# Kernel tuning notes

Hardware: AMD Instinct MI355X
Metric: run time of the kernel (lower is better)

Reference implementation:

```python
import jax, jax.numpy as jnp
import numpy as np

D_FEATURE = 1024
HEAD = 16
D_K = 64
D_V = 64
EPS = 1e-6


def setup_inputs() -> dict:
    key = jax.random.key(0)
    ks = jax.random.split(key, 12)
    B, S = 2, 2048
    s_in = 1.0 / np.sqrt(D_FEATURE)
    s_o = 1.0 / np.sqrt(HEAD * D_V)
    return {
        "q": jax.random.normal(ks[0], (B, S, D_FEATURE), jnp.float32),
        "k": jax.random.normal(ks[1], (B, S, D_FEATURE), jnp.float32),
        "v": jax.random.normal(ks[2], (B, S, D_FEATURE), jnp.float32),
        "Wq": jax.random.uniform(ks[3], (D_FEATURE, HEAD * D_K), jnp.float32, -s_in, s_in),
        "bq": jnp.zeros((HEAD * D_K,), jnp.float32),
        "Wk": jax.random.uniform(ks[4], (D_FEATURE, HEAD * D_K), jnp.float32, -s_in, s_in),
        "bk": jnp.zeros((HEAD * D_K,), jnp.float32),
        "Wv": jax.random.uniform(ks[5], (D_FEATURE, HEAD * D_V), jnp.float32, -s_in, s_in),
        "bv": jnp.zeros((HEAD * D_V,), jnp.float32),
        "Wo": jax.random.uniform(ks[6], (HEAD * D_V, D_FEATURE), jnp.float32, -s_o, s_o),
        "bo": jnp.zeros((D_FEATURE,), jnp.float32),
        "gamma": jnp.ones((D_FEATURE,), jnp.float32),
        "beta": jnp.zeros((D_FEATURE,), jnp.float32),
    }


def reference(q, k, v, Wq, bq, Wk, bk, Wv, bv, Wo, bo, gamma, beta):
    B, Sq, _ = q.shape
    Sk, Sv = k.shape[1], v.shape[1]
    shortcut = v
    # projections -> (b, h, s, d)
    qh = (q @ Wq + bq).reshape(B, Sq, HEAD, D_K).transpose(0, 2, 1, 3)
    kh = (k @ Wk + bk).reshape(B, Sk, HEAD, D_K).transpose(0, 2, 1, 3)
    vh = (v @ Wv + bv).reshape(B, Sv, HEAD, D_V).transpose(0, 2, 1, 3)
    scale = 1.0 / np.sqrt(D_K).astype(np.float32)
    scores = jnp.einsum('bhqd,bhkd->bhqk', qh * scale, kh)
    attn = jax.nn.softmax(scores, axis=-1)  # dropout is identity (p=0 / eval)
    ctx = jnp.einsum('bhqk,bhkd->bhqd', attn, vh)
    ctx = ctx.transpose(0, 2, 1, 3).reshape(B, Sv, HEAD * D_V)
    out = ctx @ Wo + bo
    out = out + shortcut
    # LayerNorm, eps=1e-6
    mu = out.mean(-1, keepdims=True)
    var = out.var(-1, keepdims=True)
    out = (out - mu) * jax.lax.rsqrt(var + EPS) * gamma + beta
    return out
```

## Files before the change

### kernel.cpp

```cpp
#include <hip/hip_runtime.h>

#define D_FEAT 1024
#define NTOK   4096
#define SEQ    2048
#define NHEAD  16
#define DK     64
#define QSCALE 0.1803368801111204f

typedef float          f32x4  __attribute__((ext_vector_type(4)));
typedef float          f32x16 __attribute__((ext_vector_type(16)));
typedef short          s16x8  __attribute__((ext_vector_type(8)));
typedef unsigned short u16x4  __attribute__((ext_vector_type(4)));

__device__ __forceinline__ unsigned short f2bf(float f) {
  union { float f; unsigned int u; } x; x.f = f;
  unsigned int r = x.u + 0x7fffu + ((x.u >> 16) & 1u);
  return (unsigned short)(r >> 16);
}
__device__ __forceinline__ unsigned short f2h(float f) {
  union { _Float16 h; unsigned short u; } x; x.h = (_Float16)f; return x.u;
}
__device__ __forceinline__ float h2f(unsigned short u) {
  union { _Float16 h; unsigned short u; } x; x.u = u; return (float)x.h;
}

__device__ __forceinline__ f32x4 mfma16(s16x8 a, s16x8 b, f32x4 c) {
  return __builtin_amdgcn_mfma_f32_16x16x32_bf16(a, b, c, 0, 0, 0);
}
__device__ __forceinline__ f32x16 mfma32(s16x8 a, s16x8 b, f32x16 c) {
  return __builtin_amdgcn_mfma_f32_32x32x16_bf16(a, b, c, 0, 0, 0);
}

__device__ __forceinline__ void gload16(const void* g, void* l) {
  __builtin_amdgcn_global_load_lds(
      (const __attribute__((address_space(1))) void*)g,
      (__attribute__((address_space(3))) void*)l, 16, 0, 0);
}

__device__ __forceinline__ float fexp2(float x) {
  return __builtin_amdgcn_exp2f(x);
}

__device__ __forceinline__ unsigned int cvtpk(float a, float b) {
  unsigned int r;
  asm("v_cvt_pk_bf16_f32 %0, %1, %2" : "=v"(r) : "v"(a), "v"(b));
  return r;
}
__device__ __forceinline__ void swap32(unsigned int& x, unsigned int& y) {
  asm("v_permlane32_swap_b32 %0, %1" : "+v"(x), "+v"(y));
}
__device__ __forceinline__ s16x8 mk8(unsigned int a, unsigned int b,
                                     unsigned int c, unsigned int d) {
  union { unsigned int u[4]; s16x8 v; } x;
  x.u[0] = a; x.u[1] = b; x.u[2] = c; x.u[3] = d; return x.v;
}

__global__ __launch_bounds__(256) void prep_kernel(
    const float* __restrict__ q, const float* __restrict__ k, const float* __restrict__ v,
    const float* __restrict__ Wq, const float* __restrict__ Wk,
    const float* __restrict__ Wv, const float* __restrict__ Wo,
    unsigned short* __restrict__ qb, unsigned short* __restrict__ kb,
    unsigned short* __restrict__ vb,
    unsigned short* __restrict__ WT, unsigned short* __restrict__ Wot)
{
  __shared__ float tile[32][33];
  const int bx = blockIdx.x, tid = threadIdx.x;
  if (bx < 12288) {
    int sel = bx >> 12;
    const float* src = sel == 0 ? q : (sel == 1 ? k : v);
    unsigned short* dst = sel == 0 ? qb : (sel == 1 ? kb : vb);
    size_t i = ((size_t)(bx & 4095) * 256 + tid) * 4;
    float4 f = *(const float4*)(src + i);
    u16x4 o; o.x = f2bf(f.x); o.y = f2bf(f.y); o.z = f2bf(f.z); o.w = f2bf(f.w);
    *(u16x4*)(dst + i) = o;
  } else {
    int t = bx - 12288;
    int z = t >> 10, rest = t & 1023;
    int bxt = rest & 31, byt = rest >> 5;
    const float* W = z == 0 ? Wq : z == 1 ? Wk : z == 2 ? Wv : Wo;
    unsigned short* T = (z < 3) ? (WT + (size_t)z * 1024 * 1024) : Wot;
    int tx = tid & 31, ty = tid >> 5;
    int n = bxt * 32 + tx;
    for (int i = 0; i < 4; ++i) {
      int kk = byt * 32 + ty + i * 8;
      tile[ty + i * 8][tx] = W[(size_t)kk * D_FEAT + n];
    }
    __syncthreads();
    int kk = byt * 32 + tx;
    for (int i = 0; i < 4; ++i) {
      int n2 = bxt * 32 + ty + i * 8;
      T[(size_t)n2 * D_FEAT + kk] = f2bf(tile[tx][ty + i * 8]);
    }
  }
}

__global__ __launch_bounds__(256, 3) void gemm_qkv(
    const unsigned short* __restrict__ qb, const unsigned short* __restrict__ kb,
    const unsigned short* __restrict__ vb, const unsigned short* __restrict__ WT,
    const float* __restrict__ bq, const float* __restrict__ bk, const float* __restrict__ bv,
    unsigned short* __restrict__ Qp, unsigned short* __restrict__ Kp, unsigned short* __restrict__ Vt)
{
  __shared__ __align__(16) unsigned short sAB[2 * 128 * 64];
  unsigned short* sA = sAB;
  unsigned short* sB = sAB + 128 * 64;
  const int tid = threadIdx.x;
  const int wave = tid >> 6, lane = tid & 63;
  const int quad = lane >> 4, l16 = lane & 15;
  const int wx = wave & 1, wy = wave >> 1;
  const int bx = blockIdx.x;
  const int chunk = bx >> 3;

  const unsigned short* rA;
  const unsigned short* rB;
  int m0, n0;
  if (chunk < 2) {
    m0 = blockIdx.y * 128; n0 = (bx & 7) * 128;
    rA = (chunk ? kb : qb) + (size_t)m0 * D_FEAT;
    rB = WT + (size_t)(chunk * 1024 + n0) * D_FEAT;
  } else {
    m0 = (bx & 7) * 128; n0 = blockIdx.y * 128;
    rA = WT + (size_t)(2048 + m0) * D_FEAT;
    rB = vb + (size_t)n0 * D_FEAT;
  }

  f32x4 acc[4][4];
  for (int mt = 0; mt < 4; ++mt)
    for (int nt = 0; nt < 4; ++nt) acc[mt][nt] = (f32x4){0.f, 0.f, 0.f, 0.f};

  const int rw8 = lane >> 3;
  const int cls = ((lane & 7) ^ (lane >> 3)) * 8;
  const int sw = l16 & 7;

  for (int k0 = 0; k0 < D_FEAT; k0 += 64) {
    __syncthreads();
    for (int j = 0; j < 4; ++j) {
      int ch = wave * 4 + j;
      gload16(rA + (size_t)(ch * 8 + rw8) * D_FEAT + k0 + cls, sA + ch * 512);
      gload16(rB + (size_t)(ch * 8 + rw8) * D_FEAT + k0 + cls, sB + ch * 512);
    }
    __syncthreads();
    s16x8 af[2][4], bfr[2][4];
    for (int kk = 0; kk < 2; ++kk) {
      int c = ((kk * 4 + quad) ^ sw) * 8;
      for (int mt = 0; mt < 4; ++mt)
        af[kk][mt] = *(const s16x8*)(sA + (wy * 64 + mt * 16 + l16) * 64 + c);
      for (int nt = 0; nt < 4; ++nt)
        bfr[kk][nt] = *(const s16x8*)(sB + (wx * 64 + nt * 16 + l16) * 64 + c);
    }
    for (int kk = 0; kk < 2; ++kk)
      for (int mt = 0; mt < 4; ++mt)
        for (int nt = 0; nt < 4; ++nt)
          acc[mt][nt] = mfma16(af[kk][mt], bfr[kk][nt], acc[mt][nt]);
  }

  if (chunk < 2) {
    const float* bias = chunk ? bk : bq;
    unsigned short* Cp = chunk ? Kp : Qp;
    const float scale = chunk == 0 ? QSCALE : 1.0f;
    for (int mt = 0; mt < 4; ++mt)
      for (int nt = 0; nt < 4; ++nt) {
        int col = n0 + wx * 64 + nt * 16 + l16;
        float bcol = bias[col];
        for (int r = 0; r < 4; ++r) {
          int row = m0 + wy * 64 + mt * 16 + quad * 4 + r;
          Cp[(size_t)row * D_FEAT + col] = f2bf((acc[mt][nt][r] + bcol) * scale);
        }
      }
  } else {
    for (int mt = 0; mt < 4; ++mt)
      for (int r = 0; r < 4; ++r) {
        float bfeat = bv[m0 + wy * 64 + mt * 16 + quad * 4 + r];
        for (int nt = 0; nt < 4; ++nt) acc[mt][nt][r] += bfeat;
      }
    unsigned short* tb = sAB;
    for (int p = 0; p < 2; ++p) {
      __syncthreads();
      if (wx == p) {
        for (int mt = 0; mt < 4; ++mt)
          for (int nt = 0; nt < 4; ++nt) {
            int tok_loc = nt * 16 + l16;
            for (int r = 0; r < 4; ++r) {
              int f_loc = wy * 64 + mt * 16 + quad * 4 + r;
              tb[f_loc * 72 + tok_loc] = f2bf(acc[mt][nt][r]);
            }
          }
      }
      __syncthreads();
      int n_base = n0 + p * 64;
      int b = n_base >> 11, tok0 = n_base & 2047;
      int ck = lane & 7;
      for (int j = 0; j < 4; ++j) {
        int f_loc = (wave * 4 + j) * 8 + rw8;
        int f = m0 + f_loc, hh = f >> 6, dv = f & 63;
        *(s16x8*)(Vt + ((size_t)(b * 16 + hh) * 64 + dv) * SEQ + tok0 + ck * 8) =
            *(const s16x8*)(tb + f_loc * 72 + ck * 8);
      }
    }
  }
}

__global__ __launch_bounds__(256) void gemm_o(
    const unsigned short* __restrict__ A, const unsigned short* __restrict__ Bt,
    const float* __restrict__ bias, const float* __restrict__ resid,
    float* __restrict__ Cout)
{
  __shared__ __align__(16) unsigned short sA[128 * 64];
  __shared__ __align__(16) unsigned short sB[64 * 64];
  const int tid = threadIdx.x;
  const int wave = tid >> 6, lane = tid & 63;
  const int quad = lane >> 4, l16 = lane & 15;
  const int wx = wave & 1, wy = wave >> 1;
  const int n0 = blockIdx.x * 64, m0 = blockIdx.y * 128;

  f32x4 acc[4][2];
  for (int mt = 0; mt < 4; ++mt)
    for (int nt = 0; nt < 2; ++nt) acc[mt][nt] = (f32x4){0.f, 0.f, 0.f, 0.f};

  const int rw8 = lane >> 3;
  const int cls = ((lane & 7) ^ (lane >> 3)) * 8;
  const int sw = l16 & 7;

  for (int k0 = 0; k0 < D_FEAT; k0 += 64) {
    __syncthreads();
    for (int j = 0; j < 4; ++j) {
      int ch = wave * 4 + j;
      gload16(A + (size_t)(m0 + ch * 8 + rw8) * D_FEAT + k0 + cls, sA + ch * 512);
    }
    for (int j = 0; j < 2; ++j) {
      int ch = wave * 2 + j;
      gload16(Bt + (size_t)(n0 + ch * 8 + rw8) * D_FEAT + k0 + cls, sB + ch * 512);
    }
    __syncthreads();
    s16x8 af[2][4], bfr[2][2];
    for (int kk = 0; kk < 2; ++kk) {
      int c = ((kk * 4 + quad) ^ sw) * 8;
      for (int mt = 0; mt < 4; ++mt)
        af[kk][mt] = *(const s16x8*)(sA + (wy * 64 + mt * 16 + l16) * 64 + c);
      for (int nt = 0; nt < 2; ++nt)
        bfr[kk][nt] = *(const s16x8*)(sB + (wx * 32 + nt * 16 + l16) * 64 + c);
    }
    for (int kk = 0; kk < 2; ++kk)
      for (int mt = 0; mt < 4; ++mt)
        for (int nt = 0; nt < 2; ++nt)
          acc[mt][nt] = mfma16(af[kk][mt], bfr[kk][nt], acc[mt][nt]);
  }

  for (int mt = 0; mt < 4; ++mt)
    for (int nt = 0; nt < 2; ++nt) {
      int col = n0 + wx * 32 + nt * 16 + l16;
      float bcol = bias[col];
      for (int r = 0; r < 4; ++r) {
        int row = m0 + wy * 64 + mt * 16 + quad * 4 + r;
        Cout[(size_t)row * D_FEAT + col] =
            acc[mt][nt][r] + bcol + resid[(size_t)row * D_FEAT + col];
      }
    }
}

__global__ __launch_bounds__(256, 3) void flash_part(
    const unsigned short* __restrict__ Qp,
    const unsigned short* __restrict__ Kp,
    const unsigned short* __restrict__ Vt,
    unsigned short* __restrict__ Opart,
    float* __restrict__ L)
{
  __shared__ __align__(16) unsigned short sB4[4][4096];

  const int tid = threadIdx.x;
  const int wave = tid >> 6, lane = tid & 63;
  const int l32 = lane & 31, h = lane >> 5;

  const int blk = blockIdx.x;
  const int xcd = blk & 7, jj = blk >> 3;
  const int grp = xcd * 8 + (jj >> 4);
  const int q0 = (jj & 15) * 128;
  const int bh = grp & 31, z = grp >> 5;
  const int b = bh >> 4, hd = bh & 15;
  const int kbase = z * (SEQ / 2);
  const size_t base = (size_t)b * SEQ * D_FEAT + (size_t)hd * DK;
  const unsigned short* vt = Vt + (size_t)bh * 64 * SEQ;

  const int qrow = wave * 32 + l32;

  const unsigned short* qptr = Qp + base + (size_t)(q0 + qrow) * D_FEAT;
  s16x8 bq[4];
#pragma unroll
  for (int s = 0; s < 4; ++s)
    bq[s] = *(const s16x8*)(qptr + (2 * s + h) * 8);

  const int krow = tid >> 3;
  const unsigned short* kPtr =
      Kp + base + (size_t)(kbase + krow) * D_FEAT + (((tid & 7) ^ (krow & 7)) * 8);
  const int vrow = tid >> 2;
  const unsigned short* vPtr =
      vt + (size_t)vrow * SEQ + kbase + (((tid & 3) ^ ((tid >> 3) & 3)) * 8);

  const int kdst = wave * 512;
#pragma unroll
  for (int pb = 0; pb < 2; ++pb) {
    gload16(kPtr, &sB4[pb][kdst]);
    gload16(vPtr, &sB4[pb][2048 + kdst]);
    kPtr += 32 * D_FEAT; vPtr += 32;
  }

  f32x16 o0, o1, stE, stO;
#pragma unroll
  for (int r = 0; r < 16; ++r) { o0[r] = 0.f; o1[r] = 0.f; }
  float lsA = 0.f, lsB = 0.f;

  const int kxor = l32 & 7;
  const int vxor = (l32 >> 1) & 3;

#define QK_TILE(BUF, ST)                                                       \
  {                                                                            \
    const unsigned short* bK = &sB4[BUF][0];                                   \
    _Pragma("unroll") for (int r = 0; r < 16; ++r) ST[r] = 0.f;                \
    __builtin_amdgcn_s_setprio(1);                                            \
    _Pragma("unroll") for (int s = 0; s < 4; ++s) {                            \
      s16x8 a = *(const s16x8*)(bK + l32 * 64 + (((2 * s + h) ^ kxor) * 8));   \
      ST = mfma32(a, bq[s], ST);                                               \
    }                                                                          \
    __builtin_amdgcn_s_setprio(0);                                            \
  }

#define SMPV_TILE(BUFV, ST)                                                    \
  {                                                                            \
    const unsigned short* bV = &sB4[BUFV][2048];                               \
    unsigned int c[8];                                                         \
    _Pragma("unroll") for (int i = 0; i < 8; ++i) {                            \
      float e0 = fexp2(ST[2 * i]);                                             \
      float e1 = fexp2(ST[2 * i + 1]);                                         \
      lsA += e0; lsB += e1;                                                    \
      c[i] = cvtpk(e0, e1);                                                    \
    }                                                                          \
    swap32(c[0], c[2]); swap32(c[1], c[3]);                                    \
    swap32(c[4], c[6]); swap32(c[5], c[7]);                                    \
    s16x8 bp0 = mk8(c[0], c[1], c[2], c[3]);                  \
    s16x8 bp1 = mk8(c[4], c[5], c[6], c[7]);                  \
    __builtin_amdgcn_s_setprio(1);                                            \
    _Pragma("unroll") for (int kk = 0; kk < 2; ++kk) {                         \
      int cs = ((2 * kk + h) ^ vxor) * 8;                                      \
      s16x8 av0 = *(const s16x8*)(bV + l32 * 32 + cs);                         \
      s16x8 av1 = *(const s16x8*)(bV + (32 + l32) * 32 + cs);                  \
      s16x8 bp = kk ? bp1 : bp0;                                               \
      o0 = mfma32(av0, bp, o0);                                                \
      o1 = mfma32(av1, bp, o1);                                                \
    }                                                                          \
    __builtin_amdgcn_s_setprio(0);                                            \
  }

#define SYNC2                                                                  \
  asm volatile("s_waitcnt vmcnt(2)" ::: "memory");                             \
  __builtin_amdgcn_s_barrier();                                               \
  __builtin_amdgcn_sched_barrier(0);
#define ISSUE(NXT)                                                             \
  gload16(kPtr, &sB4[NXT][kdst]);                                              \
  gload16(vPtr, &sB4[NXT][2048 + kdst]);                                       \
  kPtr += 32 * D_FEAT; vPtr += 32;

  SYNC2; ISSUE(2); QK_TILE(0, stE);
  SYNC2; ISSUE(3); QK_TILE(1, stO); SMPV_TILE(0, stE);
  SYNC2; ISSUE(0); QK_TILE(2, stE); SMPV_TILE(1, stO);
  SYNC2; ISSUE(1); QK_TILE(3, stO); SMPV_TILE(2, stE);
  for (int g6 = 0; g6 < 6; ++g6) {
    SYNC2; ISSUE(2); QK_TILE(0, stE); SMPV_TILE(3, stO);
    SYNC2; ISSUE(3); QK_TILE(1, stO); SMPV_TILE(0, stE);
    SYNC2; ISSUE(0); QK_TILE(2, stE); SMPV_TILE(1, stO);
    SYNC2; ISSUE(1); QK_TILE(3, stO); SMPV_TILE(2, stE);
  }
  SYNC2; ISSUE(2); QK_TILE(0, stE); SMPV_TILE(3, stO);
  SYNC2; ISSUE(3); QK_TILE(1, stO); SMPV_TILE(0, stE);
  SYNC2;           QK_TILE(2, stE); SMPV_TILE(1, stO);
  asm volatile("s_waitcnt vmcnt(0)" ::: "memory");
  __builtin_amdgcn_s_barrier();
  __builtin_amdgcn_sched_barrier(0);
  QK_TILE(3, stO); SMPV_TILE(2, stE);
  SMPV_TILE(3, stO);
#undef QK_TILE
#undef SMPV_TILE
#undef SYNC2
#undef ISSUE

  float lsum = lsA + lsB;
  lsum += __shfl_xor(lsum, 32, 64);
  const size_t trow = (size_t)(z * 32 + bh) * SEQ + (q0 + qrow);
  unsigned short* orow = Opart + trow * 64;
#pragma unroll
  for (int g = 0; g < 4; ++g) {
    u16x4 ov;
    for (int r = 0; r < 4; ++r) ov[r] = f2h(o0[4 * g + r]);
    *(u16x4*)(orow + 8 * g + 4 * h) = ov;
  }
#pragma unroll
  for (int g = 0; g < 4; ++g) {
    u16x4 ov;
    for (int r = 0; r < 4; ++r) ov[r] = f2h(o1[4 * g + r]);
    *(u16x4*)(orow + 32 + 8 * g + 4 * h) = ov;
  }
  if (h == 0) L[trow] = lsum;
}

__global__ __launch_bounds__(256) void combine_kernel(
    const unsigned short* __restrict__ Opart, const float* __restrict__ L,
    unsigned short* __restrict__ ctx)
{
  const int idx = blockIdx.x * 256 + threadIdx.x;
  const int dq = idx & 15;
  const int trow = idx >> 4;
  const int bh = trow >> 11, tok = trow & 2047;
  const int b = bh >> 4, h = bh & 15;
  const int HS = 32 * SEQ;

  float inv = __builtin_amdgcn_rcpf(L[trow] + L[HS + trow]);

  u16x4 p0 = *(const u16x4*)(Opart + (size_t)trow * 64 + dq * 4);
  u16x4 p1 = *(const u16x4*)(Opart + ((size_t)HS + trow) * 64 + dq * 4);
  u16x4 o;
  for (int r = 0; r < 4; ++r)
    o[r] = f2bf((h2f(p0[r]) + h2f(p1[r])) * inv);
  *(u16x4*)(ctx + (size_t)b * SEQ * D_FEAT + (size_t)tok * D_FEAT + h * 64 + dq * 4) = o;
}

__global__ __launch_bounds__(256) void ln_kernel(
    const float* __restrict__ x, const float* __restrict__ gamma,
    const float* __restrict__ beta, float* __restrict__ out)
{
  const int row = blockIdx.x, tid = threadIdx.x;
  const int wave = tid >> 6, lane = tid & 63;
  const float* xr = x + (size_t)row * D_FEAT;
  float4 v = ((const float4*)xr)[tid];
  float s  = v.x + v.y + v.z + v.w;
  float ss = v.x * v.x + v.y * v.y + v.z * v.z + v.w * v.w;
  for (int off = 1; off < 64; off <<= 1) {
    s  += __shfl_xor(s,  off, 64);
    ss += __shfl_xor(ss, off, 64);
  }
  __shared__ float red[8];
  if (lane == 0) { red[wave] = s; red[wave + 4] = ss; }
  __syncthreads();
  s  = red[0] + red[1] + red[2] + red[3];
  ss = red[4] + red[5] + red[6] + red[7];
  float mean = s * (1.f / D_FEAT);
  float var  = ss * (1.f / D_FEAT) - mean * mean;
  float rstd = rsqrtf(var + 1e-6f);
  float4 g  = ((const float4*)gamma)[tid];
  float4 bt = ((const float4*)beta)[tid];
  float4 o;
  o.x = (v.x - mean) * rstd * g.x + bt.x;
  o.y = (v.y - mean) * rstd * g.y + bt.y;
  o.z = (v.z - mean) * rstd * g.z + bt.z;
  o.w = (v.w - mean) * rstd * g.w + bt.w;
  ((float4*)(out + (size_t)row * D_FEAT))[tid] = o;
}

extern "C" void kernel_launch(void* const* d_in, const int* in_sizes, int n_in,
                              void* d_out, int out_size, void* d_ws, size_t ws_size,
                              hipStream_t stream) {
  const float* q     = (const float*)d_in[0];
  const float* k     = (const float*)d_in[1];
  const float* v     = (const float*)d_in[2];
  const float* Wq    = (const float*)d_in[3];
  const float* bq    = (const float*)d_in[4];
  const float* Wk    = (const float*)d_in[5];
  const float* bk    = (const float*)d_in[6];
  const float* Wv    = (const float*)d_in[7];
  const float* bv    = (const float*)d_in[8];
  const float* Wo    = (const float*)d_in[9];
  const float* bo    = (const float*)d_in[10];
  const float* gamma = (const float*)d_in[11];
  const float* beta  = (const float*)d_in[12];

  char* w = (char*)d_ws;
  const size_t MB = 1u << 20;
  unsigned short* qb    = (unsigned short*)(w + 0 * MB);
  unsigned short* kb    = (unsigned short*)(w + 8 * MB);
  unsigned short* vb    = (unsigned short*)(w + 16 * MB);
  unsigned short* WT    = (unsigned short*)(w + 24 * MB);
  unsigned short* Wot   = (unsigned short*)(w + 30 * MB);
  unsigned short* Qp    = (unsigned short*)(w + 32 * MB);
  unsigned short* Kp    = (unsigned short*)(w + 40 * MB);
  unsigned short* Vt    = (unsigned short*)(w + 48 * MB);
  unsigned short* ctx   = (unsigned short*)(w + 56 * MB);
  float*          tmp   = (float*)(w + 64 * MB);
  unsigned short* Opart = (unsigned short*)(w + 0 * MB);
  float*          L     = (float*)(w + 16 * MB);

  prep_kernel<<<16384, 256, 0, stream>>>(q, k, v, Wq, Wk, Wv, Wo, qb, kb, vb, WT, Wot);

  gemm_qkv<<<dim3(24, 32), 256, 0, stream>>>(qb, kb, vb, WT, bq, bk, bv, Qp, Kp, Vt);

  flash_part<<<1024, 256, 0, stream>>>(Qp, Kp, Vt, Opart, L);

  combine_kernel<<<4096, 256, 0, stream>>>(Opart, L, ctx);

  gemm_o<<<dim3(16, 32), 256, 0, stream>>>(ctx, Wot, bo, v, tmp);

  ln_kernel<<<NTOK, 256, 0, stream>>>(tmp, gamma, beta, (float*)d_out);
}
```

Baseline: 230.2 us.

## Double-buffer LDS tiles in QKV and output projection GEMMs

Both the QKV projection and output projection GEMMs now keep two LDS buffers. The global-to-LDS loads for the next K tile are issued while the current tile is being computed, and partial vmcnt waits replace full __syncthreads pairs. The aim is to hide global load latency behind MFMA work. In exchange, shared memory per block doubles, and the QKV kernel's launch bound drops from 3 to 2 blocks per CU, which reduces occupancy.

```diff
diff --git a/kernel.cpp b/kernel.cpp
--- a/kernel.cpp
+++ b/kernel.cpp
@@ -94,15 +94,13 @@
   }
 }
 
-__global__ __launch_bounds__(256, 3) void gemm_qkv(
+__global__ __launch_bounds__(256, 2) void gemm_qkv(
     const unsigned short* __restrict__ qb, const unsigned short* __restrict__ kb,
     const unsigned short* __restrict__ vb, const unsigned short* __restrict__ WT,
     const float* __restrict__ bq, const float* __restrict__ bk, const float* __restrict__ bv,
     unsigned short* __restrict__ Qp, unsigned short* __restrict__ Kp, unsigned short* __restrict__ Vt)
 {
-  __shared__ __align__(16) unsigned short sAB[2 * 128 * 64];
-  unsigned short* sA = sAB;
-  unsigned short* sB = sAB + 128 * 64;
+  __shared__ __align__(16) unsigned short sAB[2][2 * 128 * 64];
   const int tid = threadIdx.x;
   const int wave = tid >> 6, lane = tid & 63;
   const int quad = lane >> 4, l16 = lane & 15;
@@ -131,27 +129,59 @@
   const int cls = ((lane & 7) ^ (lane >> 3)) * 8;
   const int sw = l16 & 7;
 
-  for (int k0 = 0; k0 < D_FEAT; k0 += 64) {
-    __syncthreads();
-    for (int j = 0; j < 4; ++j) {
-      int ch = wave * 4 + j;
-      gload16(rA + (size_t)(ch * 8 + rw8) * D_FEAT + k0 + cls, sA + ch * 512);
-      gload16(rB + (size_t)(ch * 8 + rw8) * D_FEAT + k0 + cls, sB + ch * 512);
-    }
-    __syncthreads();
-    s16x8 af[2][4], bfr[2][4];
-    for (int kk = 0; kk < 2; ++kk) {
-      int c = ((kk * 4 + quad) ^ sw) * 8;
-      for (int mt = 0; mt < 4; ++mt)
-        af[kk][mt] = *(const s16x8*)(sA + (wy * 64 + mt * 16 + l16) * 64 + c);
-      for (int nt = 0; nt < 4; ++nt)
-        bfr[kk][nt] = *(const s16x8*)(sB + (wx * 64 + nt * 16 + l16) * 64 + c);
-    }
-    for (int kk = 0; kk < 2; ++kk)
-      for (int mt = 0; mt < 4; ++mt)
-        for (int nt = 0; nt < 4; ++nt)
-          acc[mt][nt] = mfma16(af[kk][mt], bfr[kk][nt], acc[mt][nt]);
-  }
+#define QKV_ISSUE(BUF, K0)                                                     \
+  _Pragma("unroll") for (int j = 0; j < 4; ++j) {                              \
+    int ch = wave * 4 + j;                                                     \
+    gload16(rA + (size_t)(ch * 8 + rw8) * D_FEAT + (K0) + cls,                 \
+            &sAB[BUF][ch * 512]);                                              \
+    gload16(rB + (size_t)(ch * 8 + rw8) * D_FEAT + (K0) + cls,                 \
+            &sAB[BUF][128 * 64 + ch * 512]);                                   \
+  }
+
+#define QKV_COMP(BUF)                                                         \
+  {                                                                            \
+    const unsigned short* sA = &sAB[BUF][0];                                   \
+    const unsigned short* sB = &sAB[BUF][128 * 64];                            \
+    s16x8 af[2][4], bfr[2][4];                                                 \
+    _Pragma("unroll") for (int kk = 0; kk < 2; ++kk) {                         \
+      int c = ((kk * 4 + quad) ^ sw) * 8;                                      \
+      _Pragma("unroll") for (int mt = 0; mt < 4; ++mt)                         \
+        af[kk][mt] = *(const s16x8*)(sA + (wy * 64 + mt * 16 + l16) * 64 + c); \
+      _Pragma("unroll") for (int nt = 0; nt < 4; ++nt)                         \
+        bfr[kk][nt] = *(const s16x8*)(sB + (wx * 64 + nt * 16 + l16) * 64 + c);\
+    }                                                                          \
+    _Pragma("unroll") for (int kk = 0; kk < 2; ++kk)                           \
+      _Pragma("unroll") for (int mt = 0; mt < 4; ++mt)                         \
+        _Pragma("unroll") for (int nt = 0; nt < 4; ++nt)                       \
+          acc[mt][nt] = mfma16(af[kk][mt], bfr[kk][nt], acc[mt][nt]);          \
+  }
+
+#define GSYNC(N)                                                               \
+  asm volatile("s_waitcnt vmcnt(" #N ")" ::: "memory");                        \
+  __builtin_amdgcn_s_barrier();                                               \
+  __builtin_amdgcn_sched_barrier(0);
+
+  QKV_ISSUE(0, 0);
+  QKV_ISSUE(1, 64);
+  for (int t2 = 0; t2 < 14; t2 += 2) {
+    GSYNC(8);
+    QKV_COMP(0);
+    __builtin_amdgcn_s_barrier();
+    __builtin_amdgcn_sched_barrier(0);
+    QKV_ISSUE(0, (t2 + 2) * 64);
+    GSYNC(8);
+    QKV_COMP(1);
+    __builtin_amdgcn_s_barrier();
+    __builtin_amdgcn_sched_barrier(0);
+    QKV_ISSUE(1, (t2 + 3) * 64);
+  }
+  GSYNC(8);
+  QKV_COMP(0);
+  GSYNC(0);
+  QKV_COMP(1);
+#undef QKV_ISSUE
+#undef QKV_COMP
+#undef GSYNC
 
   if (chunk < 2) {
     const float* bias = chunk ? bk : bq;
@@ -172,7 +202,7 @@
         float bfeat = bv[m0 + wy * 64 + mt * 16 + quad * 4 + r];
         for (int nt = 0; nt < 4; ++nt) acc[mt][nt][r] += bfeat;
       }
-    unsigned short* tb = sAB;
+    unsigned short* tb = &sAB[0][0];
     for (int p = 0; p < 2; ++p) {
       __syncthreads();
       if (wx == p) {
@@ -204,8 +234,8 @@
     const float* __restrict__ bias, const float* __restrict__ resid,
     float* __restrict__ Cout)
 {
-  __shared__ __align__(16) unsigned short sA[128 * 64];
-  __shared__ __align__(16) unsigned short sB[64 * 64];
+  __shared__ __align__(16) unsigned short sA2[2][128 * 64];
+  __shared__ __align__(16) unsigned short sB2[2][64 * 64];
   const int tid = threadIdx.x;
   const int wave = tid >> 6, lane = tid & 63;
   const int quad = lane >> 4, l16 = lane & 15;
@@ -220,30 +250,62 @@
   const int cls = ((lane & 7) ^ (lane >> 3)) * 8;
   const int sw = l16 & 7;
 
-  for (int k0 = 0; k0 < D_FEAT; k0 += 64) {
-    __syncthreads();
-    for (int j = 0; j < 4; ++j) {
-      int ch = wave * 4 + j;
-      gload16(A + (size_t)(m0 + ch * 8 + rw8) * D_FEAT + k0 + cls, sA + ch * 512);
-    }
-    for (int j = 0; j < 2; ++j) {
-      int ch = wave * 2 + j;
-      gload16(Bt + (size_t)(n0 + ch * 8 + rw8) * D_FEAT + k0 + cls, sB + ch * 512);
-    }
-    __syncthreads();
-    s16x8 af[2][4], bfr[2][2];
-    for (int kk = 0; kk < 2; ++kk) {
-      int c = ((kk * 4 + quad) ^ sw) * 8;
-      for (int mt = 0; mt < 4; ++mt)
-        af[kk][mt] = *(const s16x8*)(sA + (wy * 64 + mt * 16 + l16) * 64 + c);
-      for (int nt = 0; nt < 2; ++nt)
-        bfr[kk][nt] = *(const s16x8*)(sB + (wx * 32 + nt * 16 + l16) * 64 + c);
-    }
-    for (int kk = 0; kk < 2; ++kk)
-      for (int mt = 0; mt < 4; ++mt)
-        for (int nt = 0; nt < 2; ++nt)
-          acc[mt][nt] = mfma16(af[kk][mt], bfr[kk][nt], acc[mt][nt]);
-  }
+#define O_ISSUE(BUF, K0)                                                       \
+  _Pragma("unroll") for (int j = 0; j < 4; ++j) {                              \
+    int ch = wave * 4 + j;                                                     \
+    gload16(A + (size_t)(m0 + ch * 8 + rw8) * D_FEAT + (K0) + cls,             \
+            &sA2[BUF][ch * 512]);                                              \
+  }                                                                            \
+  _Pragma("unroll") for (int j = 0; j < 2; ++j) {                              \
+    int ch = wave * 2 + j;                                                     \
+    gload16(Bt + (size_t)(n0 + ch * 8 + rw8) * D_FEAT + (K0) + cls,            \
+            &sB2[BUF][ch * 512]);                                              \
+  }
+
+#define O_COMP(BUF)                                                           \
+  {                                                                            \
+    const unsigned short* sA = &sA2[BUF][0];                                   \
+    const unsigned short* sB = &sB2[BUF][0];                                   \
+    s16x8 af[2][4], bfr[2][2];                                                 \
+    _Pragma("unroll") for (int kk = 0; kk < 2; ++kk) {                         \
+      int c = ((kk * 4 + quad) ^ sw) * 8;                                      \
+      _Pragma("unroll") for (int mt = 0; mt < 4; ++mt)                         \
+        af[kk][mt] = *(const s16x8*)(sA + (wy * 64 + mt * 16 + l16) * 64 + c); \
+      _Pragma("unroll") for (int nt = 0; nt < 2; ++nt)                         \
+        bfr[kk][nt] = *(const s16x8*)(sB + (wx * 32 + nt * 16 + l16) * 64 + c);\
+    }                                                                          \
+    _Pragma("unroll") for (int kk = 0; kk < 2; ++kk)                           \
+      _Pragma("unroll") for (int mt = 0; mt < 4; ++mt)                         \
+        _Pragma("unroll") for (int nt = 0; nt < 2; ++nt)                       \
+          acc[mt][nt] = mfma16(af[kk][mt], bfr[kk][nt], acc[mt][nt]);          \
+  }
+
+#define GSYNC(N)                                                               \
+  asm volatile("s_waitcnt vmcnt(" #N ")" ::: "memory");                        \
+  __builtin_amdgcn_s_barrier();                                               \
+  __builtin_amdgcn_sched_barrier(0);
+
+  O_ISSUE(0, 0);
+  O_ISSUE(1, 64);
+  for (int t2 = 0; t2 < 14; t2 += 2) {
+    GSYNC(6);
+    O_COMP(0);
+    __builtin_amdgcn_s_barrier();
+    __builtin_amdgcn_sched_barrier(0);
+    O_ISSUE(0, (t2 + 2) * 64);
+    GSYNC(6);
+    O_COMP(1);
+    __builtin_amdgcn_s_barrier();
+    __builtin_amdgcn_sched_barrier(0);
+    O_ISSUE(1, (t2 + 3) * 64);
+  }
+  GSYNC(6);
+  O_COMP(0);
+  GSYNC(0);
+  O_COMP(1);
+#undef O_ISSUE
+#undef O_COMP
+#undef GSYNC
 
   for (int mt = 0; mt < 4; ++mt)
     for (int nt = 0; nt < 2; ++nt) {
@@ -335,8 +397,8 @@
     }                                                                          \
     swap32(c[0], c[2]); swap32(c[1], c[3]);                                    \
     swap32(c[4], c[6]); swap32(c[5], c[7]);                                    \
-    s16x8 bp0 = mk8(c[0], c[1], c[2], c[3]);                  \
-    s16x8 bp1 = mk8(c[4], c[5], c[6], c[7]);                  \
+    s16x8 bp0 = mk8(c[0], c[1], c[2], c[3]);                                   \
+    s16x8 bp1 = mk8(c[4], c[5], c[6], c[7]);                                   \
     __builtin_amdgcn_s_setprio(1);                                            \
     _Pragma("unroll") for (int kk = 0; kk < 2; ++kk) {                         \
       int cs = ((2 * kk + h) ^ vxor) * 8;                                      \
```

After: 227.8 us. No clear change (-1.0%).
